# Performance work log

Measured on AMD Instinct MI355X. Metric: run time of the kernel, lower is better.

The kernel has to match this reference:

```python
import jax, jax.numpy as jnp
import numpy as np

N = 50000
E = 200000
IN = 165
HID = 100
H1, H2, H3 = 8, 8, 1
NC = 2
DIM1 = HID * H1  # 800
DIM2 = HID * H2  # 800
NEG_SLOPE = 0.2


def setup_inputs() -> dict:
    key = jax.random.key(0)
    ks = jax.random.split(key, 20)
    p = lambda k, shape: jax.random.normal(k, shape, jnp.float32) * 0.05
    x = jax.random.normal(ks[0], (N, IN), jnp.float32)
    edge_index = jax.random.randint(ks[1], (2, E), 0, N, jnp.int64)
    return {
        "x": x,
        "edge_index": edge_index,
        "W1": p(ks[2], (IN, H1 * HID)), "a1s": p(ks[3], (H1, HID)),
        "a1d": p(ks[4], (H1, HID)), "b1": jnp.zeros((H1 * HID,), jnp.float32),
        "W2": p(ks[5], (DIM1, H2 * HID)), "a2s": p(ks[6], (H2, HID)),
        "a2d": p(ks[7], (H2, HID)), "b2": jnp.zeros((H2 * HID,), jnp.float32),
        # gat3: 800 -> 2, 1 head, mean (concat=False)
        "W3": p(ks[8], (DIM2, H3 * NC)), "a3s": p(ks[9], (H3, NC)),
        "a3d": p(ks[10], (H3, NC)), "b3": jnp.zeros((NC,), jnp.float32),
        # residual / skip linears (bias=False), stored [in, out]
        "Wres1": p(ks[11], (DIM1, DIM2)),
        "Wres2": p(ks[12], (DIM2, NC)),
        "Wskip": p(ks[13], (IN, NC)),
    }


def gat_conv(x, W, a_src, a_dst, b, src, dst, n, heads, ch, concat):
    # h: [n, heads, ch] projected node features
    h = (x @ W).reshape(n, heads, ch)
    e_src = (h * a_src).sum(-1)  # [n, heads]
    e_dst = (h * a_dst).sum(-1)
    # per-edge attention logits, LeakyReLU as in PyG GATConv
    e = jax.nn.leaky_relu(e_src[src] + e_dst[dst], NEG_SLOPE)  # [Etot, heads]
    # segment softmax over incoming edges of each destination node
    m = jax.ops.segment_max(e, dst, num_segments=n)
    ex = jnp.exp(e - m[dst])
    denom = jax.ops.segment_sum(ex, dst, num_segments=n)
    alpha = ex / (denom[dst] + 1e-16)
    # weighted scatter-aggregation of source messages
    out = jax.ops.segment_sum(alpha[:, :, None] * h[src], dst, num_segments=n)
    out = out.reshape(n, heads * ch) if concat else out.mean(axis=1)
    return out + b


def reference(x, edge_index, W1, a1s, a1d, b1, W2, a2s, a2d, b2,
              W3, a3s, a3d, b3, Wres1, Wres2, Wskip):
    n = x.shape[0]
    loop = jnp.arange(n, dtype=edge_index.dtype)  # PyG adds self-loops by default
    src = jnp.concatenate([edge_index[0], loop])
    dst = jnp.concatenate([edge_index[1], loop])

    h1 = jax.nn.elu(gat_conv(x, W1, a1s, a1d, b1, src, dst, n, H1, HID, True))
    h2 = gat_conv(h1, W2, a2s, a2d, b2, src, dst, n, H2, HID, True) + h1 @ Wres1
    h2 = jax.nn.elu(h2)
    logits = gat_conv(h2, W3, a3s, a3d, b3, src, dst, n, H3, NC, False)
    logits = logits + h2 @ Wres2 + x @ Wskip
    return logits
```

## Files before the change

kernel.cpp:

```cpp
#include <hip/hip_runtime.h>

#define NN     50000
#define NE     200000
#define ETOT   250000
#define FIN    165
#define KP1    192
#define HEADS  8
#define CH     100
#define DIM    800
#define MPAD   50048
#define NP1    896
#define DIM2   1600
#define NP2    1664
#define NEG    0.2f

typedef unsigned short u16;
typedef unsigned int   u32;
typedef __bf16 bf16x8 __attribute__((ext_vector_type(8)));
typedef float  f32x4  __attribute__((ext_vector_type(4)));

__device__ __forceinline__ u16 f2b(float f) {
  u32 u = __float_as_uint(f);
  u = (u + 0x7FFFu + ((u >> 16) & 1u)) >> 16;
  return (u16)u;
}
__device__ __forceinline__ float b2f(u16 u) { return __uint_as_float(((u32)u) << 16); }

__global__ void k_count(const int* __restrict__ ei, int* __restrict__ cnt) {
  int e = blockIdx.x * 256 + threadIdx.x;
  if (e >= ETOT) return;
  int d = (e < NE) ? ei[NE + e] : (e - NE);
  atomicAdd(&cnt[d], 1);
}
__global__ void k_bsum(const int* __restrict__ cnt, int* __restrict__ bs) {
  __shared__ int sm[256];
  int i = blockIdx.x * 256 + threadIdx.x;
  sm[threadIdx.x] = (i < NN) ? cnt[i] : 0;
  __syncthreads();
  for (int off = 128; off; off >>= 1) {
    if (threadIdx.x < off) sm[threadIdx.x] += sm[threadIdx.x + off];
    __syncthreads();
  }
  if (!threadIdx.x) bs[blockIdx.x] = sm[0];
}
__global__ void k_top(int* __restrict__ bs, int* __restrict__ rs, int nb) {
  __shared__ int sm[256];
  int t = threadIdx.x;
  int v = (t < nb) ? bs[t] : 0;
  sm[t] = v; __syncthreads();
  for (int off = 1; off < 256; off <<= 1) {
    int add = (t >= off) ? sm[t - off] : 0;
    __syncthreads();
    sm[t] += add;
    __syncthreads();
  }
  if (t < nb) bs[t] = sm[t] - v;
  if (!t) rs[NN] = ETOT;
}
__global__ void k_scan(const int* __restrict__ cnt, const int* __restrict__ bs, int* __restrict__ rs) {
  __shared__ int sm[256];
  int t = threadIdx.x, i = blockIdx.x * 256 + t;
  int v = (i < NN) ? cnt[i] : 0;
  sm[t] = v; __syncthreads();
  for (int off = 1; off < 256; off <<= 1) {
    int add = (t >= off) ? sm[t - off] : 0;
    __syncthreads();
    sm[t] += add;
    __syncthreads();
  }
  if (i < NN) rs[i] = bs[blockIdx.x] + sm[t] - v;
}
__global__ void k_fill(const int* __restrict__ ei, const int* __restrict__ rs,
                       int* __restrict__ cur, int* __restrict__ esrc) {
  int e = blockIdx.x * 256 + threadIdx.x;
  if (e >= ETOT) return;
  int s, d;
  if (e < NE) { s = ei[e]; d = ei[NE + e]; } else { s = d = e - NE; }
  int pos = atomicAdd(&cur[d], 1);
  esrc[rs[d] + pos] = s;
}

__global__ void k_cvt_x(const float* __restrict__ x, u16* __restrict__ A) {
  int idx = blockIdx.x * 256 + threadIdx.x;
  int r = idx / KP1, k = idx - r * KP1;
  float v = (r < NN && k < FIN) ? x[r * FIN + k] : 0.f;
  A[idx] = f2b(v);
}
__global__ void k_cvt_w1(const float* __restrict__ W1, u16* __restrict__ Bt) {
  int idx = blockIdx.x * 256 + threadIdx.x;
  int j = idx / KP1, k = idx - j * KP1;
  float v = (j < DIM && k < FIN) ? W1[k * DIM + j] : 0.f;
  Bt[idx] = f2b(v);
}
__global__ void k_cvt_w2(const float* __restrict__ W2, const float* __restrict__ Wr1,
                         u16* __restrict__ Bt) {
  int idx = blockIdx.x * 256 + threadIdx.x;
  int j = idx / DIM, k = idx - j * DIM;
  float v = 0.f;
  if (j < DIM) v = W2[k * DIM + j];
  else if (j < 2 * DIM) v = Wr1[k * DIM + (j - DIM)];
  Bt[idx] = f2b(v);
}
__global__ void k_wa(const float* __restrict__ W, const float* __restrict__ as,
                     const float* __restrict__ ad, u16* __restrict__ Wt,
                     int Kin, int Kpad, int Dsp) {
  int idx = blockIdx.x * 256 + threadIdx.x;
  if (idx >= 16 * Kpad) return;
  int j = idx / Kpad, k = idx - j * Kpad;
  int h = j & 7;
  const float* a = ((j < 8) ? as : ad) + h * CH;
  float s = 0.f;
  if (k < Kin) {
    const float* wr = W + (size_t)k * DIM + h * CH;
    for (int c = 0; c < CH; ++c) s += wr[c] * a[c];
  }
  Wt[(size_t)(Dsp + j) * Kpad + k] = f2b(s);
}

__device__ __forceinline__ void gl_lds16(const u16* g, u16* l) {
  __builtin_amdgcn_global_load_lds((const __attribute__((address_space(1))) void*)g,
                                   (__attribute__((address_space(3))) void*)l, 16, 0, 0);
}

__global__ __launch_bounds__(256) void k_gemm(const u16* __restrict__ A, const u16* __restrict__ Bt,
                                              u16* __restrict__ C, float* __restrict__ es,
                                              float* __restrict__ ed, int ksteps, int K,
                                              int Dsplit, int Nreal, int ldC) {
  __shared__ __align__(16) u16 lA[2][128 * 32];
  __shared__ __align__(16) u16 lB[2][128 * 32];
  int t = threadIdx.x;
  int lane = t & 63, wv = t >> 6;

  int nwg = gridDim.x * gridDim.y;
  int h = blockIdx.y * gridDim.x + blockIdx.x;
  int q = nwg >> 3, r8 = nwg & 7;
  int xcd = h & 7, i8 = h >> 3;
  int ln = (xcd < r8 ? xcd * (q + 1) : r8 * (q + 1) + (xcd - r8) * q) + i8;
  int tn = (ln % gridDim.x) * 128, tm = (ln / gridDim.x) * 128;

  int wr = (wv >> 1) * 64, wc = (wv & 1) * 64;
  int rl = lane & 15, kl = (lane >> 4) * 8;
  int srow = t >> 2, scb = (t & 3) * 8;

  f32x4 acc[4][4];
#pragma unroll
  for (int i = 0; i < 4; ++i)
#pragma unroll
    for (int j = 0; j < 4; ++j) acc[i][j] = (f32x4){0.f, 0.f, 0.f, 0.f};

  auto stage = [&](int buf, int ks) {
    int k0 = ks * 32;
#pragma unroll
    for (int r = 0; r < 2; ++r) {
      int row = srow + r * 64;
      int chunk = (r * 256 + t) * 8;
      gl_lds16(A + (size_t)(tm + row) * K + k0 + scb, &lA[buf][chunk]);
      gl_lds16(Bt + (size_t)(tn + row) * K + k0 + scb, &lB[buf][chunk]);
    }
  };

  stage(0, 0);
  int cur = 0;
  for (int ks = 0; ks < ksteps; ++ks) {
    __syncthreads();
    if (ks + 1 < ksteps) stage(cur ^ 1, ks + 1);
    bf16x8 af[4], bfr[4];
#pragma unroll
    for (int i = 0; i < 4; ++i) {
      af[i]  = *(const bf16x8*)&lA[cur][(wr + i * 16 + rl) * 32 + kl];
      bfr[i] = *(const bf16x8*)&lB[cur][(wc + i * 16 + rl) * 32 + kl];
    }
#pragma unroll
    for (int i = 0; i < 4; ++i)
#pragma unroll
      for (int j = 0; j < 4; ++j)
        acc[i][j] = __builtin_amdgcn_mfma_f32_16x16x32_bf16(af[i], bfr[j], acc[i][j], 0, 0, 0);
    cur ^= 1;
  }
  int rq = (lane >> 4) * 4;
#pragma unroll
  for (int i = 0; i < 4; ++i) {
#pragma unroll
    for (int j = 0; j < 4; ++j) {
      int col = tn + wc + j * 16 + rl;
      if (col < Dsplit) {
#pragma unroll
        for (int q2 = 0; q2 < 4; ++q2) {
          int row = tm + wr + i * 16 + rq + q2;
          C[(size_t)row * ldC + col] = f2b(acc[i][j][q2]);
        }
      } else if (col < Nreal) {
        int cj = col - Dsplit;
        float* dst = (cj < 8) ? es : ed;
        int hh = cj & 7;
#pragma unroll
        for (int q2 = 0; q2 < 4; ++q2) {
          int row = tm + wr + i * 16 + rq + q2;
          dst[(size_t)row * 8 + hh] = acc[i][j][q2];
        }
      }
    }
  }
}

__global__ void k_stats(const int* __restrict__ rs, const int* __restrict__ esrc,
                        const float* __restrict__ es, const float* __restrict__ ed,
                        float* __restrict__ ex, float* __restrict__ dv) {
  int idx = blockIdx.x * 256 + threadIdx.x;
  if (idx >= NN * HEADS) return;
  int n = idx >> 3, h = idx & 7;
  int beg = rs[n], end = rs[n + 1];
  float edv = ed[idx];
  float den = 0.f;
  for (int j = beg; j < end; ++j) {
    float x = es[esrc[j] * 8 + h] + edv;
    x = x > 0.f ? x : NEG * x;
    float e = __expf(x);
    ex[j * 8 + h] = e;
    den += e;
  }
  dv[idx] = 1.f / (den + 1e-16f);
}

__global__ __launch_bounds__(256) void k_agg1(const int* __restrict__ rs, const int* __restrict__ esrc,
    const u16* __restrict__ Hp, const float* __restrict__ ex, const float* __restrict__ dv,
    const float* __restrict__ bias, u16* __restrict__ out) {
  int n = blockIdx.x, t = threadIdx.x;
  if (t >= 200) return;
  int beg = rs[n], end = rs[n + 1];
  int c = t * 4;
  int h = t / 25;
  float inv = dv[n * 8 + h];
  float a0 = 0.f, a1 = 0.f, a2 = 0.f, a3 = 0.f;
  for (int j = beg; j < end; ++j) {
    int s = esrc[j];
    float w = ex[j * 8 + h];
    ushort4 u = *(const ushort4*)(Hp + (size_t)s * DIM + c);
    a0 += w * b2f(u.x); a1 += w * b2f(u.y); a2 += w * b2f(u.z); a3 += w * b2f(u.w);
  }
  const float4 bb = *(const float4*)(bias + c);
  float v0 = a0 * inv + bb.x, v1 = a1 * inv + bb.y, v2 = a2 * inv + bb.z, v3 = a3 * inv + bb.w;
  v0 = v0 > 0.f ? v0 : __expf(v0) - 1.f;
  v1 = v1 > 0.f ? v1 : __expf(v1) - 1.f;
  v2 = v2 > 0.f ? v2 : __expf(v2) - 1.f;
  v3 = v3 > 0.f ? v3 : __expf(v3) - 1.f;
  ushort4 o;
  o.x = f2b(v0); o.y = f2b(v1); o.z = f2b(v2); o.w = f2b(v3);
  *(ushort4*)(out + (size_t)n * DIM + c) = o;
}

__global__ __launch_bounds__(256) void k_agg2f(const int* __restrict__ rs, const int* __restrict__ esrc,
    const u16* __restrict__ Hp, const float* __restrict__ ex, const float* __restrict__ dv,
    const float* __restrict__ bias, const u16* __restrict__ resid,
    const float* __restrict__ W3, const float* __restrict__ Wres2,
    const float* __restrict__ a3s, const float* __restrict__ a3d, const float* __restrict__ b3,
    const float* __restrict__ skp,
    float* __restrict__ H3p, float* __restrict__ base,
    float* __restrict__ es3, float* __restrict__ ed3) {
  int n = blockIdx.x, t = threadIdx.x;
  int lane = t & 63, wv = t >> 6;
  float p0 = 0.f, p1 = 0.f, r0 = 0.f, r1 = 0.f;
  if (t < 200) {
    int beg = rs[n], end = rs[n + 1];
    int c = t * 4;
    int h = t / 25;
    float inv = dv[n * 8 + h];
    float a0 = 0.f, a1 = 0.f, a2 = 0.f, a3 = 0.f;
    for (int j = beg; j < end; ++j) {
      int s = esrc[j];
      float w = ex[j * 8 + h];
      ushort4 u = *(const ushort4*)(Hp + (size_t)s * DIM2 + c);
      a0 += w * b2f(u.x); a1 += w * b2f(u.y); a2 += w * b2f(u.z); a3 += w * b2f(u.w);
    }
    const float4 bb = *(const float4*)(bias + c);
    ushort4 rr = *(const ushort4*)(resid + (size_t)n * DIM2 + c);
    float v0 = a0 * inv + bb.x + b2f(rr.x);
    float v1 = a1 * inv + bb.y + b2f(rr.y);
    float v2 = a2 * inv + bb.z + b2f(rr.z);
    float v3 = a3 * inv + bb.w + b2f(rr.w);
    v0 = v0 > 0.f ? v0 : __expf(v0) - 1.f;
    v1 = v1 > 0.f ? v1 : __expf(v1) - 1.f;
    v2 = v2 > 0.f ? v2 : __expf(v2) - 1.f;
    v3 = v3 > 0.f ? v3 : __expf(v3) - 1.f;
    const float4 w3a = *(const float4*)(W3 + 2 * c);
    const float4 w3b = *(const float4*)(W3 + 2 * c + 4);
    const float4 wra = *(const float4*)(Wres2 + 2 * c);
    const float4 wrb = *(const float4*)(Wres2 + 2 * c + 4);
    p0 = v0 * w3a.x + v1 * w3a.z + v2 * w3b.x + v3 * w3b.z;
    p1 = v0 * w3a.y + v1 * w3a.w + v2 * w3b.y + v3 * w3b.w;
    r0 = v0 * wra.x + v1 * wra.z + v2 * wrb.x + v3 * wrb.z;
    r1 = v0 * wra.y + v1 * wra.w + v2 * wrb.y + v3 * wrb.w;
  }
#pragma unroll
  for (int off = 32; off; off >>= 1) {
    p0 += __shfl_down(p0, off); p1 += __shfl_down(p1, off);
    r0 += __shfl_down(r0, off); r1 += __shfl_down(r1, off);
  }
  __shared__ float red[4][4];
  if (!lane) { red[wv][0] = p0; red[wv][1] = p1; red[wv][2] = r0; red[wv][3] = r1; }
  __syncthreads();
  if (!t) {
    float P0 = red[0][0] + red[1][0] + red[2][0] + red[3][0];
    float P1 = red[0][1] + red[1][1] + red[2][1] + red[3][1];
    float R0 = red[0][2] + red[1][2] + red[2][2] + red[3][2];
    float R1 = red[0][3] + red[1][3] + red[2][3] + red[3][3];
    H3p[2 * n] = P0; H3p[2 * n + 1] = P1;
    es3[n] = P0 * a3s[0] + P1 * a3s[1];
    ed3[n] = P0 * a3d[0] + P1 * a3d[1];
    base[2 * n]     = R0 + skp[2 * n]     + b3[0];
    base[2 * n + 1] = R1 + skp[2 * n + 1] + b3[1];
  }
}

__global__ __launch_bounds__(256) void k_l3x(const float* __restrict__ x,
    const float* __restrict__ Wskip, float* __restrict__ skp) {
  int wv = threadIdx.x >> 6, lane = threadIdx.x & 63;
  int n = blockIdx.x * 4 + wv;
  if (n >= NN) return;
  float s0 = 0.f, s1 = 0.f;
  const float* xr = x + (size_t)n * FIN;
  for (int c = lane; c < FIN; c += 64) {
    float v = xr[c];
    s0 += v * Wskip[2 * c]; s1 += v * Wskip[2 * c + 1];
  }
#pragma unroll
  for (int off = 32; off; off >>= 1) {
    s0 += __shfl_down(s0, off); s1 += __shfl_down(s1, off);
  }
  if (!lane) { skp[2 * n] = s0; skp[2 * n + 1] = s1; }
}

__global__ void k_l3agg(const int* __restrict__ rs, const int* __restrict__ esrc,
                        const float* __restrict__ H3p, const float* __restrict__ base,
                        const float* __restrict__ es3, const float* __restrict__ ed3,
                        float* __restrict__ out) {
  int n = blockIdx.x * 256 + threadIdx.x;
  if (n >= NN) return;
  int beg = rs[n], end = rs[n + 1];
  float edv = ed3[n];
  float den = 0.f, a0 = 0.f, a1 = 0.f;
  for (int j = beg; j < end; ++j) {
    int s = esrc[j];
    float e = es3[s] + edv;
    e = e > 0.f ? e : NEG * e;
    float exv = __expf(e);
    den += exv;
    a0 += exv * H3p[2 * s];
    a1 += exv * H3p[2 * s + 1];
  }
  float inv = 1.f / (den + 1e-16f);
  out[2 * n]     = base[2 * n]     + a0 * inv;
  out[2 * n + 1] = base[2 * n + 1] + a1 * inv;
}

extern "C" void kernel_launch(void* const* d_in, const int* in_sizes, int n_in,
                              void* d_out, int out_size, void* d_ws, size_t ws_size,
                              hipStream_t stream) {
  (void)in_sizes; (void)n_in; (void)out_size; (void)ws_size;
  const float* x    = (const float*)d_in[0];
  const int*   ei   = (const int*)d_in[1];
  const float* W1   = (const float*)d_in[2];
  const float* a1s  = (const float*)d_in[3];
  const float* a1d  = (const float*)d_in[4];
  const float* b1   = (const float*)d_in[5];
  const float* W2   = (const float*)d_in[6];
  const float* a2s  = (const float*)d_in[7];
  const float* a2d  = (const float*)d_in[8];
  const float* b2   = (const float*)d_in[9];
  const float* W3   = (const float*)d_in[10];
  const float* a3s  = (const float*)d_in[11];
  const float* a3d  = (const float*)d_in[12];
  const float* b3   = (const float*)d_in[13];
  const float* Wr1  = (const float*)d_in[14];
  const float* Wr2  = (const float*)d_in[15];
  const float* Wsk  = (const float*)d_in[16];
  float* out = (float*)d_out;

  char* w = (char*)d_ws;
  size_t off = 0;
  auto alloc = [&](size_t bytes) { void* p = w + off; off += (bytes + 255) & ~(size_t)255; return p; };
  int* cnt   = (int*)alloc((size_t)NN * 4);
  int* cur   = (int*)alloc((size_t)NN * 4);
  int* rs    = (int*)alloc((size_t)(NN + 1) * 4);
  int* bs    = (int*)alloc(256 * 4);
  int* esrc  = (int*)alloc((size_t)ETOT * 4);
  float* es  = (float*)alloc((size_t)MPAD * HEADS * 4);
  float* ed  = (float*)alloc((size_t)MPAD * HEADS * 4);
  float* exb = (float*)alloc((size_t)ETOT * HEADS * 4);
  float* dvf = (float*)alloc((size_t)NN * HEADS * 4);
  u16* W1t   = (u16*)alloc((size_t)NP1 * KP1 * 2);
  u16* W2t   = (u16*)alloc((size_t)NP2 * DIM * 2);
  float* H3p = (float*)alloc((size_t)NN * 2 * 4);
  float* base= (float*)alloc((size_t)NN * 2 * 4);
  float* es3 = (float*)alloc((size_t)NN * 4);
  float* ed3 = (float*)alloc((size_t)NN * 4);
  float* skp = (float*)alloc((size_t)NN * 2 * 4);
  u16* bufB  = (u16*)alloc((size_t)MPAD * DIM * 2);
  u16* bufA  = (u16*)alloc((size_t)MPAD * DIM2 * 2);
  u16* H1p   = bufA;
  u16* G2    = bufA;
  u16* A1    = bufA + (size_t)MPAD * DIM;

  const int nb = (NN + 255) / 256;
  const int ge = (ETOT + 255) / 256;
  const int gh = (NN * HEADS + 255) / 256;

  hipMemsetAsync(cnt, 0, (size_t)NN * 4, stream);
  hipMemsetAsync(cur, 0, (size_t)NN * 4, stream);
  k_count<<<ge, 256, 0, stream>>>(ei, cnt);
  k_bsum <<<nb, 256, 0, stream>>>(cnt, bs);
  k_top  <<<1, 256, 0, stream>>>(bs, rs, nb);
  k_scan <<<nb, 256, 0, stream>>>(cnt, bs, rs);
  k_fill <<<ge, 256, 0, stream>>>(ei, rs, cur, esrc);

  k_cvt_x <<<(MPAD * KP1) / 256, 256, 0, stream>>>(x, A1);
  k_cvt_w1<<<(NP1 * KP1) / 256, 256, 0, stream>>>(W1, W1t);
  k_wa    <<<(16 * KP1 + 255) / 256, 256, 0, stream>>>(W1, a1s, a1d, W1t, FIN, KP1, DIM);
  k_cvt_w2<<<(NP2 * DIM) / 256, 256, 0, stream>>>(W2, Wr1, W2t);
  k_wa    <<<(16 * DIM + 255) / 256, 256, 0, stream>>>(W2, a2s, a2d, W2t, DIM, DIM, DIM2);
  k_l3x   <<<(NN + 3) / 4, 256, 0, stream>>>(x, Wsk, skp);

  k_gemm<<<dim3(NP1 / 128, MPAD / 128), 256, 0, stream>>>(A1, W1t, H1p, es, ed,
                                                          KP1 / 32, KP1, DIM, DIM + 16, DIM);
  k_stats<<<gh, 256, 0, stream>>>(rs, esrc, es, ed, exb, dvf);
  k_agg1<<<NN, 256, 0, stream>>>(rs, esrc, H1p, exb, dvf, b1, bufB);

  k_gemm<<<dim3(NP2 / 128, MPAD / 128), 256, 0, stream>>>(bufB, W2t, G2, es, ed,
                                                          DIM / 32, DIM, DIM2, DIM2 + 16, DIM2);
  k_stats<<<gh, 256, 0, stream>>>(rs, esrc, es, ed, exb, dvf);
  k_agg2f<<<NN, 256, 0, stream>>>(rs, esrc, G2, exb, dvf, b2, G2 + DIM,
                                  W3, Wr2, a3s, a3d, b3, skp, H3p, base, es3, ed3);

  k_l3agg<<<nb, 256, 0, stream>>>(rs, esrc, H3p, base, es3, ed3, out);
}
```

Baseline: 525.4 us.

## Fuse attention softmax stats into aggregation kernels via shared-memory edge chunks

Removes the separate k_stats kernels and the per-edge exp/denominator buffers. Each aggregation block now loads its node's incoming edge sources in chunks of 64 into shared memory, computes the leaky-relu exp weights and accumulates per-head denominators with shared atomics, then does the weighted gather. This saves two launches and the global write and read of the edge-weight array, at the cost of extra __syncthreads per chunk and shared-memory atomics inside the aggregation blocks.

```diff
diff --git a/kernel.cpp b/kernel.cpp
--- a/kernel.cpp
+++ b/kernel.cpp
@@ -13,6 +13,7 @@
 #define DIM2   1600
 #define NP2    1664
 #define NEG    0.2f
+#define CHK    64
 
 typedef unsigned short u16;
 typedef unsigned int   u32;
@@ -203,41 +204,46 @@
   }
 }
 
-__global__ void k_stats(const int* __restrict__ rs, const int* __restrict__ esrc,
-                        const float* __restrict__ es, const float* __restrict__ ed,
-                        float* __restrict__ ex, float* __restrict__ dv) {
-  int idx = blockIdx.x * 256 + threadIdx.x;
-  if (idx >= NN * HEADS) return;
-  int n = idx >> 3, h = idx & 7;
-  int beg = rs[n], end = rs[n + 1];
-  float edv = ed[idx];
-  float den = 0.f;
-  for (int j = beg; j < end; ++j) {
-    float x = es[esrc[j] * 8 + h] + edv;
-    x = x > 0.f ? x : NEG * x;
-    float e = __expf(x);
-    ex[j * 8 + h] = e;
-    den += e;
-  }
-  dv[idx] = 1.f / (den + 1e-16f);
-}
 
 __global__ __launch_bounds__(256) void k_agg1(const int* __restrict__ rs, const int* __restrict__ esrc,
-    const u16* __restrict__ Hp, const float* __restrict__ ex, const float* __restrict__ dv,
+    const u16* __restrict__ Hp, const float* __restrict__ es, const float* __restrict__ ed,
     const float* __restrict__ bias, u16* __restrict__ out) {
+  __shared__ float sm_ex[CHK * 8];
+  __shared__ float sm_den[8];
+  __shared__ int   sm_src[CHK];
   int n = blockIdx.x, t = threadIdx.x;
-  if (t >= 200) return;
+  if (t < 8) sm_den[t] = 0.f;
   int beg = rs[n], end = rs[n + 1];
   int c = t * 4;
   int h = t / 25;
-  float inv = dv[n * 8 + h];
+  float edv = (t < 200) ? 0.f : 0.f;
   float a0 = 0.f, a1 = 0.f, a2 = 0.f, a3 = 0.f;
-  for (int j = beg; j < end; ++j) {
-    int s = esrc[j];
-    float w = ex[j * 8 + h];
-    ushort4 u = *(const ushort4*)(Hp + (size_t)s * DIM + c);
-    a0 += w * b2f(u.x); a1 += w * b2f(u.y); a2 += w * b2f(u.z); a3 += w * b2f(u.w);
-  }
+  __syncthreads();
+  for (int ch = beg; ch < end; ch += CHK) {
+    int ce = min(end, ch + CHK);
+    int m = ce - ch;
+    if (t < m) sm_src[t] = esrc[ch + t];
+    __syncthreads();
+    for (int i = t; i < m * 8; i += 256) {
+      int e8 = i >> 3, hh = i & 7;
+      float xv = es[sm_src[e8] * 8 + hh] + ed[n * 8 + hh];
+      xv = xv > 0.f ? xv : NEG * xv;
+      float e = __expf(xv);
+      sm_ex[i] = e;
+      atomicAdd(&sm_den[hh], e);
+    }
+    __syncthreads();
+    if (t < 200) {
+      for (int j = 0; j < m; ++j) {
+        float w = sm_ex[j * 8 + h];
+        ushort4 u = *(const ushort4*)(Hp + (size_t)sm_src[j] * DIM + c);
+        a0 += w * b2f(u.x); a1 += w * b2f(u.y); a2 += w * b2f(u.z); a3 += w * b2f(u.w);
+      }
+    }
+    __syncthreads();
+  }
+  if (t >= 200) return;
+  float inv = 1.f / (sm_den[h] + 1e-16f);
   const float4 bb = *(const float4*)(bias + c);
   float v0 = a0 * inv + bb.x, v1 = a1 * inv + bb.y, v2 = a2 * inv + bb.z, v3 = a3 * inv + bb.w;
   v0 = v0 > 0.f ? v0 : __expf(v0) - 1.f;
@@ -247,31 +253,55 @@
   ushort4 o;
   o.x = f2b(v0); o.y = f2b(v1); o.z = f2b(v2); o.w = f2b(v3);
   *(ushort4*)(out + (size_t)n * DIM + c) = o;
+  (void)edv;
 }
 
 __global__ __launch_bounds__(256) void k_agg2f(const int* __restrict__ rs, const int* __restrict__ esrc,
-    const u16* __restrict__ Hp, const float* __restrict__ ex, const float* __restrict__ dv,
+    const u16* __restrict__ Hp, const float* __restrict__ es, const float* __restrict__ ed,
     const float* __restrict__ bias, const u16* __restrict__ resid,
     const float* __restrict__ W3, const float* __restrict__ Wres2,
     const float* __restrict__ a3s, const float* __restrict__ a3d, const float* __restrict__ b3,
     const float* __restrict__ skp,
     float* __restrict__ H3p, float* __restrict__ base,
     float* __restrict__ es3, float* __restrict__ ed3) {
+  __shared__ float sm_ex[CHK * 8];
+  __shared__ float sm_den[8];
+  __shared__ int   sm_src[CHK];
+  __shared__ float red[4][4];
   int n = blockIdx.x, t = threadIdx.x;
   int lane = t & 63, wv = t >> 6;
+  if (t < 8) sm_den[t] = 0.f;
+  int beg = rs[n], end = rs[n + 1];
+  int c = t * 4;
+  int h = t / 25;
+  float a0 = 0.f, a1 = 0.f, a2 = 0.f, a3 = 0.f;
+  __syncthreads();
+  for (int ch = beg; ch < end; ch += CHK) {
+    int ce = min(end, ch + CHK);
+    int m = ce - ch;
+    if (t < m) sm_src[t] = esrc[ch + t];
+    __syncthreads();
+    for (int i = t; i < m * 8; i += 256) {
+      int e8 = i >> 3, hh = i & 7;
+      float xv = es[sm_src[e8] * 8 + hh] + ed[n * 8 + hh];
+      xv = xv > 0.f ? xv : NEG * xv;
+      float e = __expf(xv);
+      sm_ex[i] = e;
+      atomicAdd(&sm_den[hh], e);
+    }
+    __syncthreads();
+    if (t < 200) {
+      for (int j = 0; j < m; ++j) {
+        float w = sm_ex[j * 8 + h];
+        ushort4 u = *(const ushort4*)(Hp + (size_t)sm_src[j] * DIM2 + c);
+        a0 += w * b2f(u.x); a1 += w * b2f(u.y); a2 += w * b2f(u.z); a3 += w * b2f(u.w);
+      }
+    }
+    __syncthreads();
+  }
   float p0 = 0.f, p1 = 0.f, r0 = 0.f, r1 = 0.f;
   if (t < 200) {
-    int beg = rs[n], end = rs[n + 1];
-    int c = t * 4;
-    int h = t / 25;
-    float inv = dv[n * 8 + h];
-    float a0 = 0.f, a1 = 0.f, a2 = 0.f, a3 = 0.f;
-    for (int j = beg; j < end; ++j) {
-      int s = esrc[j];
-      float w = ex[j * 8 + h];
-      ushort4 u = *(const ushort4*)(Hp + (size_t)s * DIM2 + c);
-      a0 += w * b2f(u.x); a1 += w * b2f(u.y); a2 += w * b2f(u.z); a3 += w * b2f(u.w);
-    }
+    float inv = 1.f / (sm_den[h] + 1e-16f);
     const float4 bb = *(const float4*)(bias + c);
     ushort4 rr = *(const ushort4*)(resid + (size_t)n * DIM2 + c);
     float v0 = a0 * inv + bb.x + b2f(rr.x);
@@ -296,7 +326,6 @@
     p0 += __shfl_down(p0, off); p1 += __shfl_down(p1, off);
     r0 += __shfl_down(r0, off); r1 += __shfl_down(r1, off);
   }
-  __shared__ float red[4][4];
   if (!lane) { red[wv][0] = p0; red[wv][1] = p1; red[wv][2] = r0; red[wv][3] = r1; }
   __syncthreads();
   if (!t) {
@@ -386,8 +415,6 @@
   int* esrc  = (int*)alloc((size_t)ETOT * 4);
   float* es  = (float*)alloc((size_t)MPAD * HEADS * 4);
   float* ed  = (float*)alloc((size_t)MPAD * HEADS * 4);
-  float* exb = (float*)alloc((size_t)ETOT * HEADS * 4);
-  float* dvf = (float*)alloc((size_t)NN * HEADS * 4);
   u16* W1t   = (u16*)alloc((size_t)NP1 * KP1 * 2);
   u16* W2t   = (u16*)alloc((size_t)NP2 * DIM * 2);
   float* H3p = (float*)alloc((size_t)NN * 2 * 4);
@@ -403,7 +430,6 @@
 
   const int nb = (NN + 255) / 256;
   const int ge = (ETOT + 255) / 256;
-  const int gh = (NN * HEADS + 255) / 256;
 
   hipMemsetAsync(cnt, 0, (size_t)NN * 4, stream);
   hipMemsetAsync(cur, 0, (size_t)NN * 4, stream);
@@ -422,13 +448,11 @@
 
   k_gemm<<<dim3(NP1 / 128, MPAD / 128), 256, 0, stream>>>(A1, W1t, H1p, es, ed,
                                                           KP1 / 32, KP1, DIM, DIM + 16, DIM);
-  k_stats<<<gh, 256, 0, stream>>>(rs, esrc, es, ed, exb, dvf);
-  k_agg1<<<NN, 256, 0, stream>>>(rs, esrc, H1p, exb, dvf, b1, bufB);
+  k_agg1<<<NN, 256, 0, stream>>>(rs, esrc, H1p, es, ed, b1, bufB);
 
   k_gemm<<<dim3(NP2 / 128, MPAD / 128), 256, 0, stream>>>(bufB, W2t, G2, es, ed,
                                                           DIM / 32, DIM, DIM2, DIM2 + 16, DIM2);
-  k_stats<<<gh, 256, 0, stream>>>(rs, esrc, es, ed, exb, dvf);
-  k_agg2f<<<NN, 256, 0, stream>>>(rs, esrc, G2, exb, dvf, b2, G2 + DIM,
+  k_agg2f<<<NN, 256, 0, stream>>>(rs, esrc, G2, es, ed, b2, G2 + DIM,
                                   W3, Wr2, a3s, a3d, b3, skp, H3p, base, es3, ed3);
 
   k_l3agg<<<nb, 256, 0, stream>>>(rs, esrc, H3p, base, es3, ed3, out);
```

Measured after the change: 508.2 us. 3.3% less time.
